# Performance work log

Hardware: AMD Instinct MI355X
Metric: run time of the kernel (lower is better)

The kernel has to match this reference:

```python
import jax, jax.numpy as jnp
import numpy as np

DIM, HEADS, DFF = 768, 12, 3072
DK = DIM // HEADS
EPS = 1e-5

def _layernorm(x, w, b):
    mu = jnp.mean(x, axis=-1, keepdims=True)
    var = jnp.mean(jnp.square(x - mu), axis=-1, keepdims=True)
    return (x - mu) * jax.lax.rsqrt(var + EPS) * w + b

def setup_inputs() -> dict:
    key = jax.random.key(0)
    ks = jax.random.split(key, 5)
    B, N = 8, 1024
    std = 0.02
    return {
        "x": jax.random.normal(ks[0], (B, N, DIM), jnp.float32),
        "ln1_w": jnp.ones((DIM,), jnp.float32),
        "ln1_b": jnp.zeros((DIM,), jnp.float32),
        "qkv_w": jax.random.normal(ks[1], (3 * DIM, DIM), jnp.float32) * std,
        "qkv_b": jnp.zeros((3 * DIM,), jnp.float32),
        "proj_w": jax.random.normal(ks[2], (DIM, DIM), jnp.float32) * std,
        "proj_b": jnp.zeros((DIM,), jnp.float32),
        "ln2_w": jnp.ones((DIM,), jnp.float32),
        "ln2_b": jnp.zeros((DIM,), jnp.float32),
        "fc1_w": jax.random.normal(ks[3], (DFF, DIM), jnp.float32) * std,
        "fc1_b": jnp.zeros((DFF,), jnp.float32),
        "fc2_w": jax.random.normal(ks[4], (DIM, DFF), jnp.float32) * std,
        "fc2_b": jnp.zeros((DIM,), jnp.float32),
    }

def reference(x, ln1_w, ln1_b, qkv_w, qkv_b, proj_w, proj_b,
              ln2_w, ln2_b, fc1_w, fc1_b, fc2_w, fc2_b):
    B, N, C = x.shape
    # --- attention branch (pre-norm) ---
    h = _layernorm(x, ln1_w, ln1_b)
    qkv = h @ qkv_w.T + qkv_b                      # [B,N,3C]
    qkv = qkv.reshape(B, N, 3, HEADS, DK)
    q = qkv[:, :, 0].transpose(0, 2, 1, 3)         # [B,H,N,dk]
    k = qkv[:, :, 1].transpose(0, 2, 1, 3)
    v = qkv[:, :, 2].transpose(0, 2, 1, 3)
    scale = DK ** -0.5
    attn = jnp.einsum('bhnd,bhmd->bhnm', q, k) * scale
    attn = jax.nn.softmax(attn, axis=-1)
    out = jnp.einsum('bhnm,bhmd->bhnd', attn, v)   # [B,H,N,dk]
    out = out.transpose(0, 2, 1, 3).reshape(B, N, C)
    out = out @ proj_w.T + proj_b
    x = x + out
    # --- MLP branch (pre-norm) ---
    h = _layernorm(x, ln2_w, ln2_b)
    h = jax.nn.gelu(h @ fc1_w.T + fc1_b, approximate=False)
    h = h @ fc2_w.T + fc2_b
    return x + h
```

## Files before the change

kernel.cpp:

```cpp
#include <hip/hip_runtime.h>
#include <hip/hip_bf16.h>
#include <hip/hip_fp8.h>
#include <math.h>

typedef __attribute__((ext_vector_type(8))) __bf16 bf16x8;
typedef __attribute__((ext_vector_type(4))) __bf16 bf16x4;
typedef __attribute__((ext_vector_type(4))) float f32x4;
typedef __attribute__((ext_vector_type(4))) int i32x4;
typedef __attribute__((ext_vector_type(8))) int i32x8;

#define DIM 768
#define DFF 3072
#define HEADS 12
#define DKH 64
#define SEQ 1024
#define BATCH 8
#define ROWS (SEQ * BATCH)

#define GLD16(gp, lp)                                                      \
  __builtin_amdgcn_global_load_lds(                                        \
      (const __attribute__((address_space(1))) void*)(gp),                 \
      (__attribute__((address_space(3))) void*)(lp), 16, 0, 0)

__device__ __forceinline__ unsigned int pack4_e4m3(float a, float b, float c, float d) {
  __hip_fp8_e4m3 q0(a), q1(b), q2(c), q3(d);
  return (unsigned int)q0.__x | ((unsigned int)q1.__x << 8) |
         ((unsigned int)q2.__x << 16) | ((unsigned int)q3.__x << 24);
}

__global__ __launch_bounds__(256) void cvt4_kernel(const float* __restrict__ s0, int n0,
                                                   const float* __restrict__ s1, int n1,
                                                   const float* __restrict__ s2, int n2,
                                                   const float* __restrict__ s3, int n3,
                                                   __bf16* __restrict__ d0,
                                                   __bf16* __restrict__ d1,
                                                   unsigned char* __restrict__ d2,
                                                   unsigned char* __restrict__ d3) {
  int i0 = blockIdx.x * 256 + threadIdx.x;
  int st = gridDim.x * 256;
  const float* bsrc[2] = {s0, s1};
  __bf16* bdst[2] = {d0, d1};
  int bns[2] = {n0, n1};
#pragma unroll
  for (int t = 0; t < 2; ++t) {
    const f32x4* in = reinterpret_cast<const f32x4*>(bsrc[t]);
    bf16x4* out = reinterpret_cast<bf16x4*>(bdst[t]);
    for (int i = i0; i < bns[t]; i += st) {
      f32x4 v = in[i];
      bf16x4 o;
#pragma unroll
      for (int j = 0; j < 4; ++j) o[j] = (__bf16)v[j];
      out[i] = o;
    }
  }
  const float* fsrc[2] = {s2, s3};
  unsigned char* fdst[2] = {d2, d3};
  int fns[2] = {n2, n3};
#pragma unroll
  for (int t = 0; t < 2; ++t) {
    const f32x4* in = reinterpret_cast<const f32x4*>(fsrc[t]);
    unsigned int* out = reinterpret_cast<unsigned int*>(fdst[t]);
    for (int i = i0; i < fns[t]; i += st) {
      f32x4 v = in[i];
      out[i] = pack4_e4m3(v[0] * 16.f, v[1] * 16.f, v[2] * 16.f, v[3] * 16.f);
    }
  }
}

__global__ __launch_bounds__(256) void ln_kernel(const float* __restrict__ x,
                                                 const float* __restrict__ w,
                                                 const float* __restrict__ b,
                                                 __bf16* __restrict__ out) {
  int wid = threadIdx.x >> 6, lane = threadIdx.x & 63;
  int row = blockIdx.x * 4 + wid;
  const f32x4* xp = reinterpret_cast<const f32x4*>(x + (size_t)row * DIM);
  f32x4 v[3];
  float s1 = 0.f, s2 = 0.f;
#pragma unroll
  for (int i = 0; i < 3; ++i) {
    v[i] = xp[lane + i * 64];
#pragma unroll
    for (int c = 0; c < 4; ++c) { s1 += v[i][c]; s2 += v[i][c] * v[i][c]; }
  }
#pragma unroll
  for (int off = 1; off < 64; off <<= 1) {
    s1 += __shfl_xor(s1, off, 64);
    s2 += __shfl_xor(s2, off, 64);
  }
  float mu = s1 * (1.f / DIM);
  float var = s2 * (1.f / DIM) - mu * mu;
  float rs = rsqrtf(var + 1e-5f);
  const f32x4* wp = reinterpret_cast<const f32x4*>(w);
  const f32x4* bp = reinterpret_cast<const f32x4*>(b);
  __bf16* op = out + (size_t)row * DIM;
#pragma unroll
  for (int i = 0; i < 3; ++i) {
    int c4 = lane + i * 64;
    f32x4 wv = wp[c4], bv = bp[c4];
    bf16x4 ov;
#pragma unroll
    for (int c = 0; c < 4; ++c) ov[c] = (__bf16)((v[i][c] - mu) * rs * wv[c] + bv[c]);
    *reinterpret_cast<bf16x4*>(&op[c4 * 4]) = ov;
  }
}

__global__ __launch_bounds__(256) void ln_f8_kernel(const float* __restrict__ x,
                                                    const float* __restrict__ w,
                                                    const float* __restrict__ b,
                                                    unsigned char* __restrict__ out) {
  int wid = threadIdx.x >> 6, lane = threadIdx.x & 63;
  int row = blockIdx.x * 4 + wid;
  const f32x4* xp = reinterpret_cast<const f32x4*>(x + (size_t)row * DIM);
  f32x4 v[3];
  float s1 = 0.f, s2 = 0.f;
#pragma unroll
  for (int i = 0; i < 3; ++i) {
    v[i] = xp[lane + i * 64];
#pragma unroll
    for (int c = 0; c < 4; ++c) { s1 += v[i][c]; s2 += v[i][c] * v[i][c]; }
  }
#pragma unroll
  for (int off = 1; off < 64; off <<= 1) {
    s1 += __shfl_xor(s1, off, 64);
    s2 += __shfl_xor(s2, off, 64);
  }
  float mu = s1 * (1.f / DIM);
  float var = s2 * (1.f / DIM) - mu * mu;
  float rs = rsqrtf(var + 1e-5f);
  const f32x4* wp = reinterpret_cast<const f32x4*>(w);
  const f32x4* bp = reinterpret_cast<const f32x4*>(b);
  unsigned int* op = reinterpret_cast<unsigned int*>(out + (size_t)row * DIM);
#pragma unroll
  for (int i = 0; i < 3; ++i) {
    int c4 = lane + i * 64;
    f32x4 wv = wp[c4], bv = bp[c4];
    float o0 = (v[i][0] - mu) * rs * wv[0] + bv[0];
    float o1 = (v[i][1] - mu) * rs * wv[1] + bv[1];
    float o2 = (v[i][2] - mu) * rs * wv[2] + bv[2];
    float o3 = (v[i][3] - mu) * rs * wv[3] + bv[3];
    op[c4] = pack4_e4m3(o0, o1, o2, o3);
  }
}

template <int EPI, int BN, int DBUF>
__global__ __launch_bounds__(256) void gemm_nt(const __bf16* __restrict__ A,
                                               const __bf16* __restrict__ B,
                                               const float* __restrict__ bias,
                                               const float* __restrict__ resid,
                                               __bf16* __restrict__ vt,
                                               void* __restrict__ Cout,
                                               int M, int N, int K) {
  constexpr int NBUF = DBUF ? 2 : 1;
  constexpr int MF = (BN == 128) ? 4 : 2;
  static_assert(BN == 64, "vmcnt count assumes 6 staging loads per thread");
  __shared__ __bf16 As[NBUF * 128 * 64];
  __shared__ __bf16 Bs[NBUF * BN * 64];
  int tid = threadIdx.x;
  int bm = blockIdx.x, bn = blockIdx.y;
  int wid = tid >> 6, lane = tid & 63;
  int l15 = lane & 15, l4 = lane >> 4;
  int rowb = (BN == 128) ? (wid >> 1) * 64 : wid * 32;
  int colb = (BN == 128) ? (wid & 1) * 64 : 0;

  f32x4 acc[MF][4] = {};

  auto stage = [&](int buf, int kt) {
    __bf16* Ab = As + buf * 128 * 64;
    __bf16* Bb = Bs + buf * BN * 64;
#pragma unroll
    for (int r = 0; r < 4; ++r) {
      int c0 = (r * 4 + wid) * 64;
      int c = c0 + lane;
      int row = c >> 3;
      int colE = ((c & 7) ^ (row & 7)) * 8;
      GLD16(&A[(size_t)(bm * 128 + row) * K + kt + colE], &Ab[c0 * 8]);
    }
#pragma unroll
    for (int r = 0; r < BN / 32; ++r) {
      int c0 = (r * 4 + wid) * 64;
      int c = c0 + lane;
      int row = c >> 3;
      int colE = ((c & 7) ^ (row & 7)) * 8;
      GLD16(&B[(size_t)(bn * BN + row) * K + kt + colE], &Bb[c0 * 8]);
    }
  };

  auto compute = [&](int buf) {
    const __bf16* Ab = As + buf * 128 * 64;
    const __bf16* Bb = Bs + buf * BN * 64;
#pragma unroll
    for (int kc = 0; kc < 2; ++kc) {
      int cswz = ((kc * 4 + l4) ^ (l15 & 7)) * 8;
      bf16x8 af[MF], bfr[4];
#pragma unroll
      for (int m = 0; m < MF; ++m)
        af[m] = *reinterpret_cast<const bf16x8*>(&Ab[(rowb + m * 16 + l15) * 64 + cswz]);
#pragma unroll
      for (int n = 0; n < 4; ++n)
        bfr[n] = *reinterpret_cast<const bf16x8*>(&Bb[(colb + n * 16 + l15) * 64 + cswz]);
#pragma unroll
      for (int m = 0; m < MF; ++m)
#pragma unroll
        for (int n = 0; n < 4; ++n)
          acc[m][n] = __builtin_amdgcn_mfma_f32_16x16x32_bf16(af[m], bfr[n], acc[m][n], 0, 0, 0);
    }
  };

  if constexpr (DBUF) {
    stage(0, 0);
    int cur = 0;
    for (int kt = 0; kt < K; kt += 64) {
      if (kt + 64 < K) {
        stage(cur ^ 1, kt + 64);
        asm volatile("s_waitcnt vmcnt(6)" ::: "memory");
      } else {
        asm volatile("s_waitcnt vmcnt(0)" ::: "memory");
      }
      __builtin_amdgcn_s_barrier();
      compute(cur);
      asm volatile("s_waitcnt lgkmcnt(0)" ::: "memory");
      __builtin_amdgcn_s_barrier();
      cur ^= 1;
    }
  } else {
    for (int kt = 0; kt < K; kt += 64) {
      __syncthreads();
      stage(0, kt);
      __syncthreads();
      compute(0);
    }
  }

#pragma unroll
  for (int m = 0; m < MF; ++m)
#pragma unroll
    for (int n = 0; n < 4; ++n) {
      int row0 = bm * 128 + rowb + m * 16 + l4 * 4;
      int col = bn * BN + colb + n * 16 + l15;
      float bc = bias[col];
      if (EPI == 0 && col >= 2 * DIM) {
        int h = (col - 2 * DIM) >> 6, dk = (col - 2 * DIM) & 63;
        int b = row0 >> 10, tok = row0 & 1023;
        bf16x4 pk;
#pragma unroll
        for (int j = 0; j < 4; ++j) pk[j] = (__bf16)(acc[m][n][j] + bc);
        *reinterpret_cast<bf16x4*>(
            &vt[(size_t)((b * HEADS + h) * DKH + dk) * SEQ + tok]) = pk;
      } else {
#pragma unroll
        for (int j = 0; j < 4; ++j) {
          float v = acc[m][n][j] + bc;
          size_t idx = (size_t)(row0 + j) * N + col;
          if (EPI == 0) {
            ((__bf16*)Cout)[idx] = (__bf16)v;
          } else {
            ((float*)Cout)[idx] = v + resid[idx];
          }
        }
      }
    }
}

template <int EPI>
__global__ __launch_bounds__(256) void gemm_fp8(const unsigned char* __restrict__ A,
                                                const unsigned char* __restrict__ B,
                                                const float* __restrict__ bias,
                                                const float* __restrict__ resid,
                                                void* __restrict__ Cout,
                                                int M, int N, int K) {
  __shared__ unsigned char As[2 * 128 * 128];
  __shared__ unsigned char Bs[2 * 64 * 128];
  int tid = threadIdx.x;
  int bm = blockIdx.x, bn = blockIdx.y;
  int wid = tid >> 6, lane = tid & 63;
  int l15 = lane & 15, l4 = lane >> 4;
  int rowb = wid * 32;

  f32x4 acc[2][4] = {};

  auto stage = [&](int buf, int kt) {
    unsigned char* Ab = As + buf * 128 * 128;
    unsigned char* Bb = Bs + buf * 64 * 128;
#pragma unroll
    for (int r = 0; r < 4; ++r) {
      int c0 = (r * 4 + wid) * 64;
      int c = c0 + lane;
      int row = c >> 3;
      int j = (c & 7) ^ (row & 7);
      GLD16(&A[(size_t)(bm * 128 + row) * K + kt + j * 16], &Ab[c0 * 16]);
    }
#pragma unroll
    for (int r = 0; r < 2; ++r) {
      int c0 = (r * 4 + wid) * 64;
      int c = c0 + lane;
      int row = c >> 3;
      int j = (c & 7) ^ (row & 7);
      GLD16(&B[(size_t)(bn * 64 + row) * K + kt + j * 16], &Bb[c0 * 16]);
    }
  };

  auto ld32 = [&](const unsigned char* base, int row) -> i32x8 {
    int s7 = l15 & 7;
    i32x4 lo = *reinterpret_cast<const i32x4*>(&base[row * 128 + (((2 * l4) ^ s7) * 16)]);
    i32x4 hi = *reinterpret_cast<const i32x4*>(&base[row * 128 + (((2 * l4 + 1) ^ s7) * 16)]);
    i32x8 r;
    r[0] = lo[0]; r[1] = lo[1]; r[2] = lo[2]; r[3] = lo[3];
    r[4] = hi[0]; r[5] = hi[1]; r[6] = hi[2]; r[7] = hi[3];
    return r;
  };

  auto compute = [&](int buf) {
    const unsigned char* Ab = As + buf * 128 * 128;
    const unsigned char* Bb = Bs + buf * 64 * 128;
    i32x8 af[2], bfr[4];
#pragma unroll
    for (int m = 0; m < 2; ++m) af[m] = ld32(Ab, rowb + m * 16 + l15);
#pragma unroll
    for (int n = 0; n < 4; ++n) bfr[n] = ld32(Bb, n * 16 + l15);
#pragma unroll
    for (int m = 0; m < 2; ++m)
#pragma unroll
      for (int n = 0; n < 4; ++n)
        acc[m][n] = __builtin_amdgcn_mfma_scale_f32_16x16x128_f8f6f4(
            af[m], bfr[n], acc[m][n], 0, 0,
            0, 0x7F7F7F7F,
            0, 0x7F7F7F7F);
  };

  stage(0, 0);
  int cur = 0;
  for (int kt = 0; kt < K; kt += 128) {
    if (kt + 128 < K) {
      stage(cur ^ 1, kt + 128);
      asm volatile("s_waitcnt vmcnt(6)" ::: "memory");
    } else {
      asm volatile("s_waitcnt vmcnt(0)" ::: "memory");
    }
    __builtin_amdgcn_s_barrier();
    compute(cur);
    asm volatile("s_waitcnt lgkmcnt(0)" ::: "memory");
    __builtin_amdgcn_s_barrier();
    cur ^= 1;
  }

#pragma unroll
  for (int m = 0; m < 2; ++m)
#pragma unroll
    for (int n = 0; n < 4; ++n) {
      int row0 = bm * 128 + rowb + m * 16 + l4 * 4;
      int col = bn * 64 + n * 16 + l15;
      float bc = bias[col];
#pragma unroll
      for (int j = 0; j < 4; ++j) {
        if (EPI == 0) {
          float v = acc[m][n][j] * 0.0625f + bc;
          float z = 1.59576912f * (v + 0.044715f * v * v * v);
          float tt = __expf(fminf(z, 80.f));
          float g = v * __fdividef(tt, tt + 1.0f);
          ((unsigned char*)Cout)[(size_t)(row0 + j) * N + col] =
              __hip_fp8_e4m3(g * 16.f).__x;
        } else {
          size_t idx = (size_t)(row0 + j) * N + col;
          ((float*)Cout)[idx] = acc[m][n][j] * (1.f / 256.f) + bc + resid[idx];
        }
      }
    }
}

__global__ __launch_bounds__(256, 3) void attn_kernel(const __bf16* __restrict__ qkv,
                                                      const __bf16* __restrict__ vt,
                                                      __bf16* __restrict__ out) {
  int bid = blockIdx.x;
  int xcd = bid & 7, kk0 = bid >> 3;
  int bh = (kk0 >> 3) * 8 + xcd;
  int qt = kk0 & 7;
  int b = bh / HEADS, h = bh % HEADS;
  int tid = threadIdx.x, wid = tid >> 6, lane = tid & 63;
  int l15 = lane & 15, l4 = lane >> 4;
  int qr0 = qt * 128 + wid * 32;
  const size_t rs = 3 * DIM;
  const __bf16* Qb = qkv + (size_t)(b * SEQ) * rs + h * DKH;
  const __bf16* Kb = Qb + DIM;
  const __bf16* Vb = vt + (size_t)bh * DKH * SEQ;

  __shared__ __bf16 Ks[64 * 64];
  __shared__ __bf16 Vs[64 * 64];
  __shared__ __bf16 Ps[4][32][72];
  __bf16(*Psw)[72] = Ps[wid];

  bf16x8 qf[2][2];
#pragma unroll
  for (int m = 0; m < 2; ++m)
#pragma unroll
    for (int kc = 0; kc < 2; ++kc) {
      bf16x8 t = *reinterpret_cast<const bf16x8*>(
          &Qb[(size_t)(qr0 + m * 16 + l15) * rs + kc * 32 + l4 * 8]);
#pragma unroll
      for (int e = 0; e < 8; ++e) t[e] = (__bf16)((float)t[e] * 0.125f);
      qf[m][kc] = t;
    }

  f32x4 o[2][4] = {};
  f32x4 lsum[2] = {};

  for (int kv0 = 0; kv0 < SEQ; kv0 += 64) {
    __syncthreads();
#pragma unroll
    for (int cc = 0; cc < 2; ++cc) {
      int c0 = (wid * 2 + cc) * 64;
      int c = c0 + lane;
      int row = c >> 3;
      int sb = (c & 7) * 16;
      int pkc = sb ^ (((row >> 2) & 7) << 4);
      GLD16(&Kb[(size_t)(kv0 + row) * rs + (pkc >> 1)], &Ks[c0 * 8]);
      int pvc = sb ^ ((row & 7) << 4);
      GLD16(&Vb[(size_t)row * SEQ + kv0 + (pvc >> 1)], &Vs[c0 * 8]);
    }
    __syncthreads();

    bf16x8 kb[4][2];
#pragma unroll
    for (int nf = 0; nf < 4; ++nf)
#pragma unroll
      for (int kc = 0; kc < 2; ++kc) {
        int row = 4 * l15 + nf;
        int col = (kc * 64 + l4 * 16) ^ ((l15 & 7) << 4);
        kb[nf][kc] = *reinterpret_cast<const bf16x8*>(&Ks[row * 64 + (col >> 1)]);
      }
    f32x4 s[2][4] = {};
#pragma unroll
    for (int m = 0; m < 2; ++m)
#pragma unroll
      for (int nf = 0; nf < 4; ++nf)
#pragma unroll
        for (int kc = 0; kc < 2; ++kc)
          s[m][nf] = __builtin_amdgcn_mfma_f32_16x16x32_bf16(qf[m][kc], kb[nf][kc], s[m][nf], 0, 0, 0);

    bf16x8 vf[4][2];
#pragma unroll
    for (int d = 0; d < 4; ++d)
#pragma unroll
      for (int kc = 0; kc < 2; ++kc) {
        int row = d * 16 + l15;
        int col = (kc * 64 + l4 * 16) ^ ((l15 & 7) << 4);
        vf[d][kc] = *reinterpret_cast<const bf16x8*>(&Vs[row * 64 + (col >> 1)]);
      }

#pragma unroll
    for (int m = 0; m < 2; ++m)
#pragma unroll
      for (int j = 0; j < 4; ++j) {
        bf16x4 pk;
        float ss = 0.f;
#pragma unroll
        for (int nf = 0; nf < 4; ++nf) {
          float p = __expf(s[m][nf][j]);
          ss += p;
          pk[nf] = (__bf16)p;
        }
        lsum[m][j] += ss;
        *reinterpret_cast<bf16x4*>(&Psw[m * 16 + l4 * 4 + j][l15 * 4]) = pk;
      }
    asm volatile("s_waitcnt lgkmcnt(0)" ::: "memory");
    __builtin_amdgcn_sched_barrier(0);

    bf16x8 pf[2][2];
#pragma unroll
    for (int m = 0; m < 2; ++m)
#pragma unroll
      for (int kc = 0; kc < 2; ++kc)
        pf[m][kc] = *reinterpret_cast<const bf16x8*>(&Psw[m * 16 + l15][kc * 32 + l4 * 8]);
#pragma unroll
    for (int m = 0; m < 2; ++m)
#pragma unroll
      for (int d = 0; d < 4; ++d)
#pragma unroll
        for (int kc = 0; kc < 2; ++kc)
          o[m][d] = __builtin_amdgcn_mfma_f32_16x16x32_bf16(pf[m][kc], vf[d][kc], o[m][d], 0, 0, 0);
  }

#pragma unroll
  for (int off = 1; off < 16; off <<= 1)
#pragma unroll
    for (int m = 0; m < 2; ++m)
#pragma unroll
      for (int j = 0; j < 4; ++j) lsum[m][j] += __shfl_xor(lsum[m][j], off, 64);

  __bf16* op = out + (size_t)(b * SEQ) * DIM + h * DKH;
#pragma unroll
  for (int m = 0; m < 2; ++m)
#pragma unroll
    for (int j = 0; j < 4; ++j) {
      float rl = 1.f / lsum[m][j];
      int row = qr0 + m * 16 + l4 * 4 + j;
#pragma unroll
      for (int d = 0; d < 4; ++d)
        op[(size_t)row * DIM + d * 16 + l15] = (__bf16)(o[m][d][j] * rl);
    }
}

extern "C" void kernel_launch(void* const* d_in, const int* in_sizes, int n_in,
                              void* d_out, int out_size, void* d_ws, size_t ws_size,
                              hipStream_t stream) {
  const float* x      = (const float*)d_in[0];
  const float* ln1_w  = (const float*)d_in[1];
  const float* ln1_b  = (const float*)d_in[2];
  const float* qkv_w  = (const float*)d_in[3];
  const float* qkv_b  = (const float*)d_in[4];
  const float* proj_w = (const float*)d_in[5];
  const float* proj_b = (const float*)d_in[6];
  const float* ln2_w  = (const float*)d_in[7];
  const float* ln2_b  = (const float*)d_in[8];
  const float* fc1_w  = (const float*)d_in[9];
  const float* fc1_b  = (const float*)d_in[10];
  const float* fc2_w  = (const float*)d_in[11];
  const float* fc2_b  = (const float*)d_in[12];

  char* ws = (char*)d_ws;
  size_t o = 0;
  __bf16* qkvw_bf = (__bf16*)(ws + o); o += (size_t)3 * DIM * DIM * 2;
  __bf16* projw_bf = (__bf16*)(ws + o); o += (size_t)DIM * DIM * 2;
  unsigned char* fc1w_f8 = (unsigned char*)(ws + o); o += (size_t)DFF * DIM;
  unsigned char* fc2w_f8 = (unsigned char*)(ws + o); o += (size_t)DIM * DFF;
  __bf16* h_bf    = (__bf16*)(ws + o); o += (size_t)ROWS * DIM * 2;
  float*  x1      = (float*)(ws + o);  o += (size_t)ROWS * DIM * 4;
  __bf16* qkv_bf  = (__bf16*)(ws + o); o += (size_t)ROWS * 3 * DIM * 2;
  __bf16* attn_bf = (__bf16*)(ws + o); o += (size_t)ROWS * DIM * 2;
  unsigned char* ff_f8 = (unsigned char*)qkv_bf;
  __bf16* vtp     = (__bf16*)x1;
  unsigned char* h_f8 = (unsigned char*)h_bf;

  cvt4_kernel<<<2048, 256, 0, stream>>>(
      qkv_w, 3 * DIM * DIM / 4, proj_w, DIM * DIM / 4,
      fc1_w, DFF * DIM / 4, fc2_w, DIM * DFF / 4,
      qkvw_bf, projw_bf, fc1w_f8, fc2w_f8);

  ln_kernel<<<ROWS / 4, 256, 0, stream>>>(x, ln1_w, ln1_b, h_bf);
  gemm_nt<0, 64, 1><<<dim3(ROWS / 128, 3 * DIM / 64), 256, 0, stream>>>(
      h_bf, qkvw_bf, qkv_b, nullptr, vtp, qkv_bf, ROWS, 3 * DIM, DIM);
  attn_kernel<<<dim3(8 * BATCH * HEADS), 256, 0, stream>>>(qkv_bf, vtp, attn_bf);
  gemm_nt<2, 64, 1><<<dim3(ROWS / 128, DIM / 64), 256, 0, stream>>>(
      attn_bf, projw_bf, proj_b, x, nullptr, x1, ROWS, DIM, DIM);
  ln_f8_kernel<<<ROWS / 4, 256, 0, stream>>>(x1, ln2_w, ln2_b, h_f8);
  gemm_fp8<0><<<dim3(ROWS / 128, DFF / 64), 256, 0, stream>>>(
      h_f8, fc1w_f8, fc1_b, nullptr, ff_f8, ROWS, DFF, DIM);
  gemm_fp8<1><<<dim3(ROWS / 128, DIM / 64), 256, 0, stream>>>(
      ff_f8, fc2w_f8, fc2_b, x1, (float*)d_out, ROWS, DIM, DFF);
}
```

Measured before the change: 193.4 us.

## Enlarge GEMM tiles to 128x128 with 2x2 wave layout and unrolled double buffer

Both the bf16 and fp8 GEMMs move from 128x64 output tiles to 128x128 tiles, with the four waves arranged 2x2 so each computes a 64x64 sub-tile (16 accumulators). The goal is to raise arithmetic intensity per LDS/global load and halve the number of blocks. The K loop is unrolled by two with fixed buffer indices, and launch_bounds now asks for 2 blocks per CU. In exchange, accumulator registers and LDS per block grow, grid size halves (fewer blocks for small GEMMs like proj and fc2), and the loop assumes K is a multiple of twice the tile depth.

After: 194.1 us. No clear change (+0.3%).

```diff
diff --git a/kernel.cpp b/kernel.cpp
--- a/kernel.cpp
+++ b/kernel.cpp
@@ -142,31 +142,28 @@
   }
 }
 
-template <int EPI, int BN, int DBUF>
-__global__ __launch_bounds__(256) void gemm_nt(const __bf16* __restrict__ A,
-                                               const __bf16* __restrict__ B,
-                                               const float* __restrict__ bias,
-                                               const float* __restrict__ resid,
-                                               __bf16* __restrict__ vt,
-                                               void* __restrict__ Cout,
-                                               int M, int N, int K) {
-  constexpr int NBUF = DBUF ? 2 : 1;
-  constexpr int MF = (BN == 128) ? 4 : 2;
-  static_assert(BN == 64, "vmcnt count assumes 6 staging loads per thread");
-  __shared__ __bf16 As[NBUF * 128 * 64];
-  __shared__ __bf16 Bs[NBUF * BN * 64];
+template <int EPI>
+__global__ __launch_bounds__(256, 2) void gemm_nt(const __bf16* __restrict__ A,
+                                                  const __bf16* __restrict__ B,
+                                                  const float* __restrict__ bias,
+                                                  const float* __restrict__ resid,
+                                                  __bf16* __restrict__ vt,
+                                                  void* __restrict__ Cout,
+                                                  int M, int N, int K) {
+  __shared__ __bf16 As[2 * 128 * 64];
+  __shared__ __bf16 Bs[2 * 128 * 64];
   int tid = threadIdx.x;
   int bm = blockIdx.x, bn = blockIdx.y;
   int wid = tid >> 6, lane = tid & 63;
   int l15 = lane & 15, l4 = lane >> 4;
-  int rowb = (BN == 128) ? (wid >> 1) * 64 : wid * 32;
-  int colb = (BN == 128) ? (wid & 1) * 64 : 0;
-
-  f32x4 acc[MF][4] = {};
+  int rowb = (wid >> 1) * 64;
+  int colb = (wid & 1) * 64;
+
+  f32x4 acc[4][4] = {};
 
   auto stage = [&](int buf, int kt) {
     __bf16* Ab = As + buf * 128 * 64;
-    __bf16* Bb = Bs + buf * BN * 64;
+    __bf16* Bb = Bs + buf * 128 * 64;
 #pragma unroll
     for (int r = 0; r < 4; ++r) {
       int c0 = (r * 4 + wid) * 64;
@@ -176,67 +173,62 @@
       GLD16(&A[(size_t)(bm * 128 + row) * K + kt + colE], &Ab[c0 * 8]);
     }
 #pragma unroll
-    for (int r = 0; r < BN / 32; ++r) {
+    for (int r = 0; r < 4; ++r) {
       int c0 = (r * 4 + wid) * 64;
       int c = c0 + lane;
       int row = c >> 3;
       int colE = ((c & 7) ^ (row & 7)) * 8;
-      GLD16(&B[(size_t)(bn * BN + row) * K + kt + colE], &Bb[c0 * 8]);
+      GLD16(&B[(size_t)(bn * 128 + row) * K + kt + colE], &Bb[c0 * 8]);
     }
   };
 
   auto compute = [&](int buf) {
     const __bf16* Ab = As + buf * 128 * 64;
-    const __bf16* Bb = Bs + buf * BN * 64;
+    const __bf16* Bb = Bs + buf * 128 * 64;
 #pragma unroll
     for (int kc = 0; kc < 2; ++kc) {
       int cswz = ((kc * 4 + l4) ^ (l15 & 7)) * 8;
-      bf16x8 af[MF], bfr[4];
-#pragma unroll
-      for (int m = 0; m < MF; ++m)
+      bf16x8 af[4], bfr[4];
+#pragma unroll
+      for (int m = 0; m < 4; ++m)
         af[m] = *reinterpret_cast<const bf16x8*>(&Ab[(rowb + m * 16 + l15) * 64 + cswz]);
 #pragma unroll
       for (int n = 0; n < 4; ++n)
         bfr[n] = *reinterpret_cast<const bf16x8*>(&Bb[(colb + n * 16 + l15) * 64 + cswz]);
 #pragma unroll
-      for (int m = 0; m < MF; ++m)
+      for (int m = 0; m < 4; ++m)
 #pragma unroll
         for (int n = 0; n < 4; ++n)
           acc[m][n] = __builtin_amdgcn_mfma_f32_16x16x32_bf16(af[m], bfr[n], acc[m][n], 0, 0, 0);
     }
   };
 
-  if constexpr (DBUF) {
-    stage(0, 0);
-    int cur = 0;
-    for (int kt = 0; kt < K; kt += 64) {
-      if (kt + 64 < K) {
-        stage(cur ^ 1, kt + 64);
-        asm volatile("s_waitcnt vmcnt(6)" ::: "memory");
-      } else {
-        asm volatile("s_waitcnt vmcnt(0)" ::: "memory");
-      }
-      __builtin_amdgcn_s_barrier();
-      compute(cur);
-      asm volatile("s_waitcnt lgkmcnt(0)" ::: "memory");
-      __builtin_amdgcn_s_barrier();
-      cur ^= 1;
-    }
-  } else {
-    for (int kt = 0; kt < K; kt += 64) {
-      __syncthreads();
-      stage(0, kt);
-      __syncthreads();
-      compute(0);
-    }
-  }
-
-#pragma unroll
-  for (int m = 0; m < MF; ++m)
+  stage(0, 0);
+  for (int kt = 0; kt < K; kt += 128) {
+    stage(1, kt + 64);
+    asm volatile("s_waitcnt vmcnt(8)" ::: "memory");
+    __builtin_amdgcn_s_barrier();
+    compute(0);
+    asm volatile("s_waitcnt lgkmcnt(0)" ::: "memory");
+    __builtin_amdgcn_s_barrier();
+    if (kt + 128 < K) {
+      stage(0, kt + 128);
+      asm volatile("s_waitcnt vmcnt(8)" ::: "memory");
+    } else {
+      asm volatile("s_waitcnt vmcnt(0)" ::: "memory");
+    }
+    __builtin_amdgcn_s_barrier();
+    compute(1);
+    asm volatile("s_waitcnt lgkmcnt(0)" ::: "memory");
+    __builtin_amdgcn_s_barrier();
+  }
+
+#pragma unroll
+  for (int m = 0; m < 4; ++m)
 #pragma unroll
     for (int n = 0; n < 4; ++n) {
       int row0 = bm * 128 + rowb + m * 16 + l4 * 4;
-      int col = bn * BN + colb + n * 16 + l15;
+      int col = bn * 128 + colb + n * 16 + l15;
       float bc = bias[col];
       if (EPI == 0 && col >= 2 * DIM) {
         int h = (col - 2 * DIM) >> 6, dk = (col - 2 * DIM) & 63;
@@ -262,25 +254,26 @@
 }
 
 template <int EPI>
-__global__ __launch_bounds__(256) void gemm_fp8(const unsigned char* __restrict__ A,
-                                                const unsigned char* __restrict__ B,
-                                                const float* __restrict__ bias,
-                                                const float* __restrict__ resid,
-                                                void* __restrict__ Cout,
-                                                int M, int N, int K) {
+__global__ __launch_bounds__(256, 2) void gemm_fp8(const unsigned char* __restrict__ A,
+                                                   const unsigned char* __restrict__ B,
+                                                   const float* __restrict__ bias,
+                                                   const float* __restrict__ resid,
+                                                   void* __restrict__ Cout,
+                                                   int M, int N, int K) {
   __shared__ unsigned char As[2 * 128 * 128];
-  __shared__ unsigned char Bs[2 * 64 * 128];
+  __shared__ unsigned char Bs[2 * 128 * 128];
   int tid = threadIdx.x;
   int bm = blockIdx.x, bn = blockIdx.y;
   int wid = tid >> 6, lane = tid & 63;
   int l15 = lane & 15, l4 = lane >> 4;
-  int rowb = wid * 32;
-
-  f32x4 acc[2][4] = {};
+  int rowb = (wid >> 1) * 64;
+  int colb = (wid & 1) * 64;
+
+  f32x4 acc[4][4] = {};
 
   auto stage = [&](int buf, int kt) {
     unsigned char* Ab = As + buf * 128 * 128;
-    unsigned char* Bb = Bs + buf * 64 * 128;
+    unsigned char* Bb = Bs + buf * 128 * 128;
 #pragma unroll
     for (int r = 0; r < 4; ++r) {
       int c0 = (r * 4 + wid) * 64;
@@ -290,35 +283,35 @@
       GLD16(&A[(size_t)(bm * 128 + row) * K + kt + j * 16], &Ab[c0 * 16]);
     }
 #pragma unroll
-    for (int r = 0; r < 2; ++r) {
+    for (int r = 0; r < 4; ++r) {
       int c0 = (r * 4 + wid) * 64;
       int c = c0 + lane;
       int row = c >> 3;
       int j = (c & 7) ^ (row & 7);
-      GLD16(&B[(size_t)(bn * 64 + row) * K + kt + j * 16], &Bb[c0 * 16]);
+      GLD16(&B[(size_t)(bn * 128 + row) * K + kt + j * 16], &Bb[c0 * 16]);
     }
   };
 
   auto ld32 = [&](const unsigned char* base, int row) -> i32x8 {
-    int s7 = l15 & 7;
-    i32x4 lo = *reinterpret_cast<const i32x4*>(&base[row * 128 + (((2 * l4) ^ s7) * 16)]);
-    i32x4 hi = *reinterpret_cast<const i32x4*>(&base[row * 128 + (((2 * l4 + 1) ^ s7) * 16)]);
+    int off = ((2 * l4) ^ (l15 & 7)) * 16;
     i32x8 r;
-    r[0] = lo[0]; r[1] = lo[1]; r[2] = lo[2]; r[3] = lo[3];
-    r[4] = hi[0]; r[5] = hi[1]; r[6] = hi[2]; r[7] = hi[3];
+    *reinterpret_cast<i32x4*>(&r) =
+        *reinterpret_cast<const i32x4*>(&base[row * 128 + off]);
+    *(reinterpret_cast<i32x4*>(&r) + 1) =
+        *reinterpret_cast<const i32x4*>(&base[row * 128 + (off ^ 16)]);
     return r;
   };
 
   auto compute = [&](int buf) {
     const unsigned char* Ab = As + buf * 128 * 128;
-    const unsigned char* Bb = Bs + buf * 64 * 128;
-    i32x8 af[2], bfr[4];
-#pragma unroll
-    for (int m = 0; m < 2; ++m) af[m] = ld32(Ab, rowb + m * 16 + l15);
-#pragma unroll
-    for (int n = 0; n < 4; ++n) bfr[n] = ld32(Bb, n * 16 + l15);
-#pragma unroll
-    for (int m = 0; m < 2; ++m)
+    const unsigned char* Bb = Bs + buf * 128 * 128;
+    i32x8 af[4], bfr[4];
+#pragma unroll
+    for (int m = 0; m < 4; ++m) af[m] = ld32(Ab, rowb + m * 16 + l15);
+#pragma unroll
+    for (int n = 0; n < 4; ++n) bfr[n] = ld32(Bb, colb + n * 16 + l15);
+#pragma unroll
+    for (int m = 0; m < 4; ++m)
 #pragma unroll
       for (int n = 0; n < 4; ++n)
         acc[m][n] = __builtin_amdgcn_mfma_scale_f32_16x16x128_f8f6f4(
@@ -328,27 +321,31 @@
   };
 
   stage(0, 0);
-  int cur = 0;
-  for (int kt = 0; kt < K; kt += 128) {
-    if (kt + 128 < K) {
-      stage(cur ^ 1, kt + 128);
-      asm volatile("s_waitcnt vmcnt(6)" ::: "memory");
+  for (int kt = 0; kt < K; kt += 256) {
+    stage(1, kt + 128);
+    asm volatile("s_waitcnt vmcnt(8)" ::: "memory");
+    __builtin_amdgcn_s_barrier();
+    compute(0);
+    asm volatile("s_waitcnt lgkmcnt(0)" ::: "memory");
+    __builtin_amdgcn_s_barrier();
+    if (kt + 256 < K) {
+      stage(0, kt + 256);
+      asm volatile("s_waitcnt vmcnt(8)" ::: "memory");
     } else {
       asm volatile("s_waitcnt vmcnt(0)" ::: "memory");
     }
     __builtin_amdgcn_s_barrier();
-    compute(cur);
+    compute(1);
     asm volatile("s_waitcnt lgkmcnt(0)" ::: "memory");
     __builtin_amdgcn_s_barrier();
-    cur ^= 1;
-  }
-
-#pragma unroll
-  for (int m = 0; m < 2; ++m)
+  }
+
+#pragma unroll
+  for (int m = 0; m < 4; ++m)
 #pragma unroll
     for (int n = 0; n < 4; ++n) {
       int row0 = bm * 128 + rowb + m * 16 + l4 * 4;
-      int col = bn * 64 + n * 16 + l15;
+      int col = bn * 128 + colb + n * 16 + l15;
       float bc = bias[col];
 #pragma unroll
       for (int j = 0; j < 4; ++j) {
@@ -536,14 +533,14 @@
       qkvw_bf, projw_bf, fc1w_f8, fc2w_f8);
 
   ln_kernel<<<ROWS / 4, 256, 0, stream>>>(x, ln1_w, ln1_b, h_bf);
-  gemm_nt<0, 64, 1><<<dim3(ROWS / 128, 3 * DIM / 64), 256, 0, stream>>>(
+  gemm_nt<0><<<dim3(ROWS / 128, 3 * DIM / 128), 256, 0, stream>>>(
       h_bf, qkvw_bf, qkv_b, nullptr, vtp, qkv_bf, ROWS, 3 * DIM, DIM);
   attn_kernel<<<dim3(8 * BATCH * HEADS), 256, 0, stream>>>(qkv_bf, vtp, attn_bf);
-  gemm_nt<2, 64, 1><<<dim3(ROWS / 128, DIM / 64), 256, 0, stream>>>(
+  gemm_nt<2><<<dim3(ROWS / 128, DIM / 128), 256, 0, stream>>>(
       attn_bf, projw_bf, proj_b, x, nullptr, x1, ROWS, DIM, DIM);
   ln_f8_kernel<<<ROWS / 4, 256, 0, stream>>>(x1, ln2_w, ln2_b, h_f8);
-  gemm_fp8<0><<<dim3(ROWS / 128, DFF / 64), 256, 0, stream>>>(
+  gemm_fp8<0><<<dim3(ROWS / 128, DFF / 128), 256, 0, stream>>>(
       h_f8, fc1w_f8, fc1_b, nullptr, ff_f8, ROWS, DFF, DIM);
-  gemm_fp8<1><<<dim3(ROWS / 128, DIM / 64), 256, 0, stream>>>(
+  gemm_fp8<1><<<dim3(ROWS / 128, DIM / 128), 256, 0, stream>>>(
       ff_f8, fc2w_f8, fc2_b, x1, (float*)d_out, ROWS, DIM, DFF);
 }
```

## Load GEMM A operand directly into registers, keep only B in LDS

Applied to the files above, without the earlier changes.

Both the bf16 and fp8 GEMMs stop staging the A tile through shared memory. Each wave loads its own A rows straight from global memory into registers, double-buffered across two register sets, while B stays double-buffered in LDS via global_load_lds. The k-loop is unrolled by two to alternate register and LDS buffers, and launch bounds request more waves per CU. This cuts LDS footprint and LDS read traffic, at the cost of more vector registers and uncoalesced per-lane global loads for A. The hardcoded vmcnt(6) wait may no longer match the per-thread load count, which risks a race.

Measured after the change: 239.1 us. 1.24x slower.

```diff
diff --git a/kernel.cpp b/kernel.cpp
--- a/kernel.cpp
+++ b/kernel.cpp
@@ -142,101 +142,95 @@
   }
 }
 
-template <int EPI, int BN, int DBUF>
-__global__ __launch_bounds__(256) void gemm_nt(const __bf16* __restrict__ A,
-                                               const __bf16* __restrict__ B,
-                                               const float* __restrict__ bias,
-                                               const float* __restrict__ resid,
-                                               __bf16* __restrict__ vt,
-                                               void* __restrict__ Cout,
-                                               int M, int N, int K) {
-  constexpr int NBUF = DBUF ? 2 : 1;
-  constexpr int MF = (BN == 128) ? 4 : 2;
-  static_assert(BN == 64, "vmcnt count assumes 6 staging loads per thread");
-  __shared__ __bf16 As[NBUF * 128 * 64];
-  __shared__ __bf16 Bs[NBUF * BN * 64];
+template <int EPI>
+__global__ __launch_bounds__(256, 4) void gemm_nt(const __bf16* __restrict__ A,
+                                                  const __bf16* __restrict__ B,
+                                                  const float* __restrict__ bias,
+                                                  const float* __restrict__ resid,
+                                                  __bf16* __restrict__ vt,
+                                                  void* __restrict__ Cout,
+                                                  int M, int N, int K) {
+  __shared__ __bf16 Bs[2 * 64 * 64];
   int tid = threadIdx.x;
   int bm = blockIdx.x, bn = blockIdx.y;
   int wid = tid >> 6, lane = tid & 63;
   int l15 = lane & 15, l4 = lane >> 4;
-  int rowb = (BN == 128) ? (wid >> 1) * 64 : wid * 32;
-  int colb = (BN == 128) ? (wid & 1) * 64 : 0;
-
-  f32x4 acc[MF][4] = {};
-
-  auto stage = [&](int buf, int kt) {
-    __bf16* Ab = As + buf * 128 * 64;
-    __bf16* Bb = Bs + buf * BN * 64;
-#pragma unroll
-    for (int r = 0; r < 4; ++r) {
+  int rowb = wid * 32;
+
+  f32x4 acc[2][4] = {};
+
+  auto stageB = [&](int buf, int kt) {
+    __bf16* Bb = Bs + buf * 64 * 64;
+#pragma unroll
+    for (int r = 0; r < 2; ++r) {
       int c0 = (r * 4 + wid) * 64;
       int c = c0 + lane;
       int row = c >> 3;
       int colE = ((c & 7) ^ (row & 7)) * 8;
-      GLD16(&A[(size_t)(bm * 128 + row) * K + kt + colE], &Ab[c0 * 8]);
-    }
-#pragma unroll
-    for (int r = 0; r < BN / 32; ++r) {
-      int c0 = (r * 4 + wid) * 64;
-      int c = c0 + lane;
-      int row = c >> 3;
-      int colE = ((c & 7) ^ (row & 7)) * 8;
-      GLD16(&B[(size_t)(bn * BN + row) * K + kt + colE], &Bb[c0 * 8]);
+      GLD16(&B[(size_t)(bn * 64 + row) * K + kt + colE], &Bb[c0 * 8]);
     }
   };
 
-  auto compute = [&](int buf) {
-    const __bf16* Ab = As + buf * 128 * 64;
-    const __bf16* Bb = Bs + buf * BN * 64;
+  auto loadA = [&](bf16x8 (&af)[2][2], int kt) {
+#pragma unroll
+    for (int m = 0; m < 2; ++m)
+#pragma unroll
+      for (int kc = 0; kc < 2; ++kc)
+        af[m][kc] = *reinterpret_cast<const bf16x8*>(
+            &A[(size_t)(bm * 128 + rowb + m * 16 + l15) * K + kt + kc * 32 + l4 * 8]);
+  };
+
+  auto mfmaStep = [&](const bf16x8 (&af)[2][2], int buf) {
+    const __bf16* Bb = Bs + buf * 64 * 64;
 #pragma unroll
     for (int kc = 0; kc < 2; ++kc) {
       int cswz = ((kc * 4 + l4) ^ (l15 & 7)) * 8;
-      bf16x8 af[MF], bfr[4];
-#pragma unroll
-      for (int m = 0; m < MF; ++m)
-        af[m] = *reinterpret_cast<const bf16x8*>(&Ab[(rowb + m * 16 + l15) * 64 + cswz]);
+      bf16x8 bfr[4];
 #pragma unroll
       for (int n = 0; n < 4; ++n)
-        bfr[n] = *reinterpret_cast<const bf16x8*>(&Bb[(colb + n * 16 + l15) * 64 + cswz]);
-#pragma unroll
-      for (int m = 0; m < MF; ++m)
+        bfr[n] = *reinterpret_cast<const bf16x8*>(&Bb[(n * 16 + l15) * 64 + cswz]);
+#pragma unroll
+      for (int m = 0; m < 2; ++m)
 #pragma unroll
         for (int n = 0; n < 4; ++n)
-          acc[m][n] = __builtin_amdgcn_mfma_f32_16x16x32_bf16(af[m], bfr[n], acc[m][n], 0, 0, 0);
+          acc[m][n] = __builtin_amdgcn_mfma_f32_16x16x32_bf16(af[m][kc], bfr[n], acc[m][n], 0, 0, 0);
     }
   };
 
-  if constexpr (DBUF) {
-    stage(0, 0);
-    int cur = 0;
-    for (int kt = 0; kt < K; kt += 64) {
-      if (kt + 64 < K) {
-        stage(cur ^ 1, kt + 64);
-        asm volatile("s_waitcnt vmcnt(6)" ::: "memory");
-      } else {
-        asm volatile("s_waitcnt vmcnt(0)" ::: "memory");
-      }
-      __builtin_amdgcn_s_barrier();
-      compute(cur);
-      asm volatile("s_waitcnt lgkmcnt(0)" ::: "memory");
-      __builtin_amdgcn_s_barrier();
-      cur ^= 1;
-    }
-  } else {
-    for (int kt = 0; kt < K; kt += 64) {
-      __syncthreads();
-      stage(0, kt);
-      __syncthreads();
-      compute(0);
-    }
-  }
-
-#pragma unroll
-  for (int m = 0; m < MF; ++m)
+  bf16x8 afA[2][2], afB[2][2];
+  stageB(0, 0);
+  loadA(afA, 0);
+  for (int kt = 0; kt < K; kt += 128) {
+    if (kt + 64 < K) {
+      stageB(1, kt + 64);
+      loadA(afB, kt + 64);
+      asm volatile("s_waitcnt vmcnt(6)" ::: "memory");
+    } else {
+      asm volatile("s_waitcnt vmcnt(0)" ::: "memory");
+    }
+    __builtin_amdgcn_s_barrier();
+    mfmaStep(afA, 0);
+    asm volatile("s_waitcnt lgkmcnt(0)" ::: "memory");
+    __builtin_amdgcn_s_barrier();
+    if (kt + 128 < K) {
+      stageB(0, kt + 128);
+      loadA(afA, kt + 128);
+      asm volatile("s_waitcnt vmcnt(6)" ::: "memory");
+    } else {
+      asm volatile("s_waitcnt vmcnt(0)" ::: "memory");
+    }
+    __builtin_amdgcn_s_barrier();
+    mfmaStep(afB, 1);
+    asm volatile("s_waitcnt lgkmcnt(0)" ::: "memory");
+    __builtin_amdgcn_s_barrier();
+  }
+
+#pragma unroll
+  for (int m = 0; m < 2; ++m)
 #pragma unroll
     for (int n = 0; n < 4; ++n) {
       int row0 = bm * 128 + rowb + m * 16 + l4 * 4;
-      int col = bn * BN + colb + n * 16 + l15;
+      int col = bn * 64 + n * 16 + l15;
       float bc = bias[col];
       if (EPI == 0 && col >= 2 * DIM) {
         int h = (col - 2 * DIM) >> 6, dk = (col - 2 * DIM) & 63;
@@ -262,13 +256,12 @@
 }
 
 template <int EPI>
-__global__ __launch_bounds__(256) void gemm_fp8(const unsigned char* __restrict__ A,
-                                                const unsigned char* __restrict__ B,
-                                                const float* __restrict__ bias,
-                                                const float* __restrict__ resid,
-                                                void* __restrict__ Cout,
-                                                int M, int N, int K) {
-  __shared__ unsigned char As[2 * 128 * 128];
+__global__ __launch_bounds__(256, 3) void gemm_fp8(const unsigned char* __restrict__ A,
+                                                   const unsigned char* __restrict__ B,
+                                                   const float* __restrict__ bias,
+                                                   const float* __restrict__ resid,
+                                                   void* __restrict__ Cout,
+                                                   int M, int N, int K) {
   __shared__ unsigned char Bs[2 * 64 * 128];
   int tid = threadIdx.x;
   int bm = blockIdx.x, bn = blockIdx.y;
@@ -278,17 +271,8 @@
 
   f32x4 acc[2][4] = {};
 
-  auto stage = [&](int buf, int kt) {
-    unsigned char* Ab = As + buf * 128 * 128;
+  auto stageB = [&](int buf, int kt) {
     unsigned char* Bb = Bs + buf * 64 * 128;
-#pragma unroll
-    for (int r = 0; r < 4; ++r) {
-      int c0 = (r * 4 + wid) * 64;
-      int c = c0 + lane;
-      int row = c >> 3;
-      int j = (c & 7) ^ (row & 7);
-      GLD16(&A[(size_t)(bm * 128 + row) * K + kt + j * 16], &Ab[c0 * 16]);
-    }
 #pragma unroll
     for (int r = 0; r < 2; ++r) {
       int c0 = (r * 4 + wid) * 64;
@@ -299,24 +283,30 @@
     }
   };
 
-  auto ld32 = [&](const unsigned char* base, int row) -> i32x8 {
+  auto loadA = [&](i32x8 (&af)[2], int kt) {
+#pragma unroll
+    for (int m = 0; m < 2; ++m) {
+      const unsigned char* p =
+          &A[(size_t)(bm * 128 + rowb + m * 16 + l15) * K + kt + l4 * 32];
+      i32x4 lo = *reinterpret_cast<const i32x4*>(p);
+      i32x4 hi = *reinterpret_cast<const i32x4*>(p + 16);
+      af[m][0] = lo[0]; af[m][1] = lo[1]; af[m][2] = lo[2]; af[m][3] = lo[3];
+      af[m][4] = hi[0]; af[m][5] = hi[1]; af[m][6] = hi[2]; af[m][7] = hi[3];
+    }
+  };
+
+  auto mfmaStep = [&](const i32x8 (&af)[2], int buf) {
+    const unsigned char* Bb = Bs + buf * 64 * 128;
     int s7 = l15 & 7;
-    i32x4 lo = *reinterpret_cast<const i32x4*>(&base[row * 128 + (((2 * l4) ^ s7) * 16)]);
-    i32x4 hi = *reinterpret_cast<const i32x4*>(&base[row * 128 + (((2 * l4 + 1) ^ s7) * 16)]);
-    i32x8 r;
-    r[0] = lo[0]; r[1] = lo[1]; r[2] = lo[2]; r[3] = lo[3];
-    r[4] = hi[0]; r[5] = hi[1]; r[6] = hi[2]; r[7] = hi[3];
-    return r;
-  };
-
-  auto compute = [&](int buf) {
-    const unsigned char* Ab = As + buf * 128 * 128;
-    const unsigned char* Bb = Bs + buf * 64 * 128;
-    i32x8 af[2], bfr[4];
-#pragma unroll
-    for (int m = 0; m < 2; ++m) af[m] = ld32(Ab, rowb + m * 16 + l15);
-#pragma unroll
-    for (int n = 0; n < 4; ++n) bfr[n] = ld32(Bb, n * 16 + l15);
+    i32x8 bfr[4];
+#pragma unroll
+    for (int n = 0; n < 4; ++n) {
+      const unsigned char* rp = &Bb[(n * 16 + l15) * 128];
+      i32x4 lo = *reinterpret_cast<const i32x4*>(&rp[((2 * l4) ^ s7) * 16]);
+      i32x4 hi = *reinterpret_cast<const i32x4*>(&rp[((2 * l4 + 1) ^ s7) * 16]);
+      bfr[n][0] = lo[0]; bfr[n][1] = lo[1]; bfr[n][2] = lo[2]; bfr[n][3] = lo[3];
+      bfr[n][4] = hi[0]; bfr[n][5] = hi[1]; bfr[n][6] = hi[2]; bfr[n][7] = hi[3];
+    }
 #pragma unroll
     for (int m = 0; m < 2; ++m)
 #pragma unroll
@@ -327,20 +317,32 @@
             0, 0x7F7F7F7F);
   };
 
-  stage(0, 0);
-  int cur = 0;
-  for (int kt = 0; kt < K; kt += 128) {
+  i32x8 afA[2], afB[2];
+  stageB(0, 0);
+  loadA(afA, 0);
+  for (int kt = 0; kt < K; kt += 256) {
     if (kt + 128 < K) {
-      stage(cur ^ 1, kt + 128);
+      stageB(1, kt + 128);
+      loadA(afB, kt + 128);
       asm volatile("s_waitcnt vmcnt(6)" ::: "memory");
     } else {
       asm volatile("s_waitcnt vmcnt(0)" ::: "memory");
     }
     __builtin_amdgcn_s_barrier();
-    compute(cur);
+    mfmaStep(afA, 0);
     asm volatile("s_waitcnt lgkmcnt(0)" ::: "memory");
     __builtin_amdgcn_s_barrier();
-    cur ^= 1;
+    if (kt + 256 < K) {
+      stageB(0, kt + 256);
+      loadA(afA, kt + 256);
+      asm volatile("s_waitcnt vmcnt(6)" ::: "memory");
+    } else {
+      asm volatile("s_waitcnt vmcnt(0)" ::: "memory");
+    }
+    __builtin_amdgcn_s_barrier();
+    mfmaStep(afB, 1);
+    asm volatile("s_waitcnt lgkmcnt(0)" ::: "memory");
+    __builtin_amdgcn_s_barrier();
   }
 
 #pragma unroll
@@ -536,10 +538,10 @@
       qkvw_bf, projw_bf, fc1w_f8, fc2w_f8);
 
   ln_kernel<<<ROWS / 4, 256, 0, stream>>>(x, ln1_w, ln1_b, h_bf);
-  gemm_nt<0, 64, 1><<<dim3(ROWS / 128, 3 * DIM / 64), 256, 0, stream>>>(
+  gemm_nt<0><<<dim3(ROWS / 128, 3 * DIM / 64), 256, 0, stream>>>(
       h_bf, qkvw_bf, qkv_b, nullptr, vtp, qkv_bf, ROWS, 3 * DIM, DIM);
   attn_kernel<<<dim3(8 * BATCH * HEADS), 256, 0, stream>>>(qkv_bf, vtp, attn_bf);
-  gemm_nt<2, 64, 1><<<dim3(ROWS / 128, DIM / 64), 256, 0, stream>>>(
+  gemm_nt<2><<<dim3(ROWS / 128, DIM / 64), 256, 0, stream>>>(
       attn_bf, projw_bf, proj_b, x, nullptr, x1, ROWS, DIM, DIM);
   ln_f8_kernel<<<ROWS / 4, 256, 0, stream>>>(x1, ln2_w, ln2_b, h_f8);
   gemm_fp8<0><<<dim3(ROWS / 128, DFF / 64), 256, 0, stream>>>(
```
